# Kernel optimization log

Measured on AMD Instinct MI355X. Metric: run time of the kernel, lower is better.

## Reference

```python
import jax, jax.numpy as jnp
import numpy as np

N, D_IN, D_H, D_ATT, N_CLUSTERS, N_CLASSES = 20000, 1024, 512, 256, 10, 4


def setup_inputs() -> dict:
    key = jax.random.key(0)
    ks = jax.random.split(key, 20)
    s = 0.02
    inp = {
        "x_path": jax.random.normal(ks[0], (N, D_IN), dtype=jnp.float32),
        "cluster_id": jax.random.randint(ks[1], (N,), 0, N_CLUSTERS, dtype=jnp.int64 if jax.config.jax_enable_x64 else jnp.int32),
        # per-cluster expert MLPs (phi_i): 1024->512->512
        "W1": jax.random.normal(ks[2], (N_CLUSTERS, D_IN, D_H), dtype=jnp.float32) * s,
        "b1": jnp.zeros((N_CLUSTERS, D_H), dtype=jnp.float32),
        "W2": jax.random.normal(ks[3], (N_CLUSTERS, D_H, D_H), dtype=jnp.float32) * s,
        "b2": jnp.zeros((N_CLUSTERS, D_H), dtype=jnp.float32),
        # attention_net: fc (512->512) then gated attention (L=512, D=256, 1)
        "Wfc": jax.random.normal(ks[4], (D_H, D_H), dtype=jnp.float32) * s,
        "bfc": jnp.zeros((D_H,), dtype=jnp.float32),
        "Wa": jax.random.normal(ks[5], (D_H, D_ATT), dtype=jnp.float32) * s,
        "ba": jnp.zeros((D_ATT,), dtype=jnp.float32),
        "Wb": jax.random.normal(ks[6], (D_H, D_ATT), dtype=jnp.float32) * s,
        "bb": jnp.zeros((D_ATT,), dtype=jnp.float32),
        "Wc": jax.random.normal(ks[7], (D_ATT, 1), dtype=jnp.float32) * s,
        "bc": jnp.zeros((1,), dtype=jnp.float32),
        # rho: 512->256
        "Wrho": jax.random.normal(ks[8], (D_H, D_ATT), dtype=jnp.float32) * s,
        "brho": jnp.zeros((D_ATT,), dtype=jnp.float32),
        # classifier: 256->4
        "Wcls": jax.random.normal(ks[9], (D_ATT, N_CLASSES), dtype=jnp.float32) * s,
        "bcls": jnp.zeros((N_CLASSES,), dtype=jnp.float32),
    }
    return inp


def reference(x_path, cluster_id, W1, b1, W2, b2, Wfc, bfc, Wa, ba, Wb, bb, Wc, bc, Wrho, brho, Wcls, bcls):
    C = W1.shape[0]
    # dispatch mask [N, C]; per-cluster counts
    onehot = jax.nn.one_hot(cluster_id, C, dtype=x_path.dtype)
    counts = jnp.maximum(onehot.sum(axis=0), 1.0)  # [C]
    # per-cluster expert MLP + masked mean-pool (AdaptiveAvgPool1d(1) over instances)
    pooled = []
    for i in range(C):  # small static loop over experts
        h = jax.nn.relu(x_path @ W1[i] + b1[i])      # [N, 512]
        h = jax.nn.relu(h @ W2[i] + b2[i])           # [N, 512]
        pooled.append((onehot[:, i] @ h) / counts[i])  # masked mean -> [512]
    h_cluster = jnp.stack(pooled, axis=0)            # [C, 512]
    # attention_net: fc then gated attention
    h = jax.nn.relu(h_cluster @ Wfc + bfc)           # [C, 512]
    a = jnp.tanh(h @ Wa + ba)                        # [C, 256]
    b = jax.nn.sigmoid(h @ Wb + bb)                  # [C, 256]
    A = ((a * b) @ Wc + bc).T                        # [1, C]
    A = jax.nn.softmax(A, axis=1)
    h_path = A @ h                                   # [1, 512]
    h_path = jax.nn.relu(h_path @ Wrho + brho).squeeze()  # [256]
    logits = (h_path @ Wcls + bcls)[None, :]         # [1, 4]
    Y_hat = jnp.argmax(logits, axis=1, keepdims=True)
    hazards = jax.nn.sigmoid(logits)
    S = jnp.cumprod(1.0 - hazards, axis=1)
    return hazards, S, Y_hat
```

## Files before the change

kernel.cpp:

```cpp
#include <hip/hip_runtime.h>
#include <hip/hip_bf16.h>
#include <math.h>


#define C_NUM 10
#define D_IN 1024
#define D_H 512
#define D_ATT 256
#define N_CLS 4
#define BM 128
#define BMG 64
#define BN 128
#define BKS 64
#define NT1 (D_IN / BKS)
#define NT2 (D_H / BKS)

typedef __attribute__((ext_vector_type(8))) short short8v;
typedef __attribute__((ext_vector_type(4))) short short4v;
typedef __attribute__((ext_vector_type(4))) float f32x4;

__device__ __forceinline__ short f2bf(float f) {
    __hip_bfloat16 h = __float2bfloat16(f);
    return *reinterpret_cast<short*>(&h);
}

__device__ __forceinline__ void gload_lds16(const void* g, void* l) {
    __builtin_amdgcn_global_load_lds((const __attribute__((address_space(1))) unsigned int*)g,
                                     (__attribute__((address_space(3))) unsigned int*)l,
                                     16, 0, 0);
}

__device__ __forceinline__ int xcd_swizzle(int orig, int nwg) {
    int q = nwg >> 3, r = nwg & 7;
    int xcd = orig & 7, base = orig >> 3;
    return (xcd < r ? xcd * (q + 1) : r * (q + 1) + (xcd - r) * q) + base;
}

__global__ __launch_bounds__(256) void k_hist(const int* __restrict__ cid, int* counts, int n) {
    __shared__ int lc[C_NUM];
    int tid = threadIdx.x;
    if (tid < C_NUM) lc[tid] = 0;
    __syncthreads();
    int i = blockIdx.x * 256 + tid;
    if (i < n) atomicAdd(&lc[cid[i]], 1);
    __syncthreads();
    if (tid < C_NUM && lc[tid] > 0) atomicAdd(&counts[tid], lc[tid]);
}

__global__ __launch_bounds__(256) void k_scatter(const int* __restrict__ cid, int* cursor,
                                                 const int* __restrict__ counts,
                                                 int* bucket, int n) {
    __shared__ int lc[C_NUM];
    __shared__ int basev[C_NUM];
    __shared__ int loff[C_NUM + 1];
    int tid = threadIdx.x;
    if (tid < C_NUM) lc[tid] = 0;
    if (tid == 0) {
        int off = 0;
        for (int c2 = 0; c2 < C_NUM; ++c2) {
            loff[c2] = off;
            off += ((counts[c2] + BM - 1) / BM) * BM;
        }
        loff[C_NUM] = off;
    }
    __syncthreads();
    int i = blockIdx.x * 256 + tid;
    int c = 0, lpos = 0;
    bool valid = (i < n);
    if (valid) { c = cid[i]; lpos = atomicAdd(&lc[c], 1); }
    __syncthreads();
    if (tid < C_NUM) basev[tid] = (lc[tid] > 0) ? atomicAdd(&cursor[tid], lc[tid]) : 0;
    __syncthreads();
    if (valid) bucket[loff[c] + basev[c] + lpos] = i;
    if (blockIdx.x == 0) {
        for (int c2 = 0; c2 < C_NUM; ++c2)
            for (int p = loff[c2] + counts[c2] + tid; p < loff[c2 + 1]; p += 256)
                bucket[p] = -1;
    }
}

__global__ __launch_bounds__(256) void k_transpose2(
    const float* __restrict__ W1, short* __restrict__ Wt1,
    const float* __restrict__ W2, short* __restrict__ Wt2)
{
    __shared__ float t[64][65];
    int bid = blockIdx.x;
    const float* src; short* dst; int K, N, k0, n0;
    if (bid < C_NUM * 128) {
        int cc = bid >> 7, r = bid & 127;
        k0 = (r & 15) * 64; n0 = (r >> 4) * 64;
        src = W1 + (size_t)cc * D_IN * D_H; dst = Wt1 + (size_t)cc * D_H * D_IN;
        K = D_IN; N = D_H;
    } else {
        int idx = bid - C_NUM * 128;
        int cc = idx >> 6, r = idx & 63;
        k0 = (r & 7) * 64; n0 = (r >> 3) * 64;
        src = W2 + (size_t)cc * D_H * D_H; dst = Wt2 + (size_t)cc * D_H * D_H;
        K = D_H; N = D_H;
    }
    int tid = threadIdx.x;
    int tk = tid >> 4, tn4 = (tid & 15) * 4;
#pragma unroll
    for (int it = 0; it < 4; ++it) {
        int k = tk + it * 16;
        f32x4 v = *(const f32x4*)&src[(size_t)(k0 + k) * N + n0 + tn4];
        t[k][tn4 + 0] = v[0]; t[k][tn4 + 1] = v[1];
        t[k][tn4 + 2] = v[2]; t[k][tn4 + 3] = v[3];
    }
    __syncthreads();
    int wn = tid >> 2, kq = (tid & 3) * 16;
#pragma unroll
    for (int q = 0; q < 4; ++q) {
        int k = kq + q * 4;
        short4v o;
#pragma unroll
        for (int e = 0; e < 4; ++e) o[e] = f2bf(t[k + e][wn]);
        *(short4v*)&dst[(size_t)(n0 + wn) * K + k0 + k] = o;
    }
}

__global__ __launch_bounds__(512) void k_gemm1w(
    const float* __restrict__ x, const short* __restrict__ Wt, const float* __restrict__ b1,
    const int* __restrict__ bucket, const int* __restrict__ counts, short* __restrict__ h1)
{
    __shared__ float Asf[BMG * BKS];
    __shared__ short Bs[BN * BKS];
    __shared__ int ridx[BMG];
    __shared__ int saoff[C_NUM + 1];

    int tid = threadIdx.x;
    int wg = xcd_swizzle(blockIdx.x, gridDim.x);
    int rowStart = (wg >> 2) * BMG;
    int colStart = (wg & 3) * BN;

    if (tid == 0) {
        int off = 0;
        for (int c2 = 0; c2 < C_NUM; ++c2) {
            saoff[c2] = off;
            off += ((counts[c2] + BM - 1) / BM) * BM;
        }
        saoff[C_NUM] = off;
    }
    if (tid < BMG) ridx[tid] = bucket[rowStart + tid];
    __syncthreads();
    if (rowStart >= saoff[C_NUM]) return;
    int c = 0;
    while (c < C_NUM - 1 && rowStart >= saoff[c + 1]) ++c;

    int lane = tid & 63;
    int wid = tid >> 6;
    int wm = wid >> 2;
    int wn = wid & 3;

    const float* aq[2];
#pragma unroll
    for (int q = 0; q < 2; ++q) {
        int row = q * 32 + wid * 4 + (lane >> 4);
        int rr = ridx[row];
        int srcslot = (lane & 15) ^ (row & 15);
        aq[q] = x + (size_t)(rr < 0 ? 0 : rr) * D_IN + srcslot * 4;
    }
    int l8 = lane >> 3;
    int sslot = (lane & 7) ^ l8;
    const short* bq[2];
#pragma unroll
    for (int q = 0; q < 2; ++q) {
        int rowb = q * 64 + wid * 8 + l8;
        bq[q] = Wt + ((size_t)c * D_H + colStart + rowb) * D_IN + sslot * 8;
    }

    f32x4 acc[2][2];
#pragma unroll
    for (int i = 0; i < 2; ++i)
#pragma unroll
        for (int j = 0; j < 2; ++j)
            acc[i][j] = f32x4{0.f, 0.f, 0.f, 0.f};

    for (int k0 = 0; k0 < D_IN; k0 += BKS) {
        gload_lds16(bq[0] + k0, &Bs[(wid * 8) * BKS]);
        gload_lds16(bq[1] + k0, &Bs[(64 + wid * 8) * BKS]);
        gload_lds16(aq[0] + k0, &Asf[(wid * 4) * BKS]);
        gload_lds16(aq[1] + k0, &Asf[(32 + wid * 4) * BKS]);
        __syncthreads();
#pragma unroll
        for (int kk = 0; kk < 2; ++kk) {
            short8v af[2], bfr[2];
#pragma unroll
            for (int i = 0; i < 2; ++i) {
                int row = wm * 32 + i * 16 + (lane & 15);
                int s8 = kk * 4 + (lane >> 4);
                int p0 = (2 * s8) ^ (row & 15);
                int p1 = (2 * s8 + 1) ^ (row & 15);
                f32x4 lo = *(const f32x4*)&Asf[row * BKS + p0 * 4];
                f32x4 hi = *(const f32x4*)&Asf[row * BKS + p1 * 4];
                short8v v;
#pragma unroll
                for (int e = 0; e < 4; ++e) { v[e] = f2bf(lo[e]); v[4 + e] = f2bf(hi[e]); }
                af[i] = v;
            }
#pragma unroll
            for (int j = 0; j < 2; ++j) {
                int nn = wn * 32 + j * 16 + (lane & 15);
                int slot = (kk * 4 + (lane >> 4)) ^ (nn & 7);
                bfr[j] = *(const short8v*)&Bs[nn * BKS + slot * 8];
            }
#pragma unroll
            for (int i = 0; i < 2; ++i)
#pragma unroll
                for (int j = 0; j < 2; ++j)
                    acc[i][j] = __builtin_amdgcn_mfma_f32_16x16x32_bf16(af[i], bfr[j], acc[i][j], 0, 0, 0);
        }
        __syncthreads();
    }

    const float* bias = b1 + c * D_H;
    float bj[2];
#pragma unroll
    for (int j = 0; j < 2; ++j) bj[j] = bias[colStart + wn * 32 + j * 16 + (lane & 15)];
#pragma unroll
    for (int i = 0; i < 2; ++i) {
#pragma unroll
        for (int r = 0; r < 4; ++r) {
            int rowl = wm * 32 + i * 16 + (lane >> 4) * 4 + r;
            bool valid = (ridx[rowl] >= 0);
            size_t gro = (size_t)(rowStart + rowl) * D_H + colStart + wn * 32 + (lane & 15);
#pragma unroll
            for (int j = 0; j < 2; ++j) {
                float v = valid ? fmaxf(acc[i][j][r] + bj[j], 0.f) : 0.f;
                h1[gro + j * 16] = f2bf(v);
            }
        }
    }
}

__global__ __launch_bounds__(512) void k_gemm2w(
    const short* __restrict__ h1, const short* __restrict__ Wt, const float* __restrict__ b2,
    const int* __restrict__ bucket, const int* __restrict__ counts, float* __restrict__ pooled)
{
    __shared__ short As[BMG * BKS];
    __shared__ short Bs[BN * BKS];
    __shared__ int ridx[BMG];
    __shared__ int saoff[C_NUM + 1];

    int tid = threadIdx.x;
    int wg = xcd_swizzle(blockIdx.x, gridDim.x);
    int rowStart = (wg >> 2) * BMG;
    int colStart = (wg & 3) * BN;

    if (tid == 0) {
        int off = 0;
        for (int c2 = 0; c2 < C_NUM; ++c2) {
            saoff[c2] = off;
            off += ((counts[c2] + BM - 1) / BM) * BM;
        }
        saoff[C_NUM] = off;
    }
    if (tid < BMG) ridx[tid] = bucket[rowStart + tid];
    __syncthreads();
    if (rowStart >= saoff[C_NUM]) return;
    int c = 0;
    while (c < C_NUM - 1 && rowStart >= saoff[c + 1]) ++c;

    int lane = tid & 63;
    int wid = tid >> 6;
    int wm = wid >> 2, wn = wid & 3;

    int l8 = lane >> 3;
    int sslot = (lane & 7) ^ l8;
    const short* abase = h1 + (size_t)(rowStart + wid * 8 + l8) * D_H + sslot * 8;
    const short* bq[2];
#pragma unroll
    for (int q = 0; q < 2; ++q) {
        int rowb = q * 64 + wid * 8 + l8;
        bq[q] = Wt + ((size_t)c * D_H + colStart + rowb) * D_H + sslot * 8;
    }

    f32x4 acc[2][2];
#pragma unroll
    for (int i = 0; i < 2; ++i)
#pragma unroll
        for (int j = 0; j < 2; ++j)
            acc[i][j] = f32x4{0.f, 0.f, 0.f, 0.f};

    for (int k0 = 0; k0 < D_H; k0 += BKS) {
        gload_lds16(abase + k0, &As[(wid * 8) * BKS]);
        gload_lds16(bq[0] + k0, &Bs[(wid * 8) * BKS]);
        gload_lds16(bq[1] + k0, &Bs[(64 + wid * 8) * BKS]);
        __syncthreads();
#pragma unroll
        for (int kk = 0; kk < 2; ++kk) {
            short8v af[2], bfr[2];
#pragma unroll
            for (int i = 0; i < 2; ++i) {
                int row = wm * 32 + i * 16 + (lane & 15);
                int slot = (kk * 4 + (lane >> 4)) ^ (row & 7);
                af[i] = *(const short8v*)&As[row * BKS + slot * 8];
            }
#pragma unroll
            for (int j = 0; j < 2; ++j) {
                int nn = wn * 32 + j * 16 + (lane & 15);
                int slot = (kk * 4 + (lane >> 4)) ^ (nn & 7);
                bfr[j] = *(const short8v*)&Bs[nn * BKS + slot * 8];
            }
#pragma unroll
            for (int i = 0; i < 2; ++i)
#pragma unroll
                for (int j = 0; j < 2; ++j)
                    acc[i][j] = __builtin_amdgcn_mfma_f32_16x16x32_bf16(af[i], bfr[j], acc[i][j], 0, 0, 0);
        }
        __syncthreads();
    }

    const float* bias = b2 + c * D_H;
    float bj[2];
#pragma unroll
    for (int j = 0; j < 2; ++j) bj[j] = bias[colStart + wn * 32 + j * 16 + (lane & 15)];
    float csum[2] = {0.f, 0.f};
#pragma unroll
    for (int i = 0; i < 2; ++i) {
#pragma unroll
        for (int r = 0; r < 4; ++r) {
            int rowl = wm * 32 + i * 16 + (lane >> 4) * 4 + r;
            float m = (ridx[rowl] >= 0) ? 1.f : 0.f;
#pragma unroll
            for (int j = 0; j < 2; ++j)
                csum[j] += m * fmaxf(acc[i][j][r] + bj[j], 0.f);
        }
    }
#pragma unroll
    for (int j = 0; j < 2; ++j) {
        float s = csum[j];
        s += __shfl_xor(s, 16, 64);
        s += __shfl_xor(s, 32, 64);
        if ((lane >> 4) == 0)
            atomicAdd(&pooled[c * D_H + colStart + wn * 32 + j * 16 + lane], s);
    }
}

__global__ __launch_bounds__(256) void k_tA(
    const float* __restrict__ pooled, const int* __restrict__ counts,
    const float* __restrict__ Wfc, const float* __restrict__ bfc,
    float* __restrict__ hfc)
{
    __shared__ float hcs[C_NUM][D_H];
    __shared__ float red[4][64][C_NUM];
    int tid = threadIdx.x;
    for (int idx = tid; idx < C_NUM * D_H; idx += 256) {
        int cc = idx >> 9;
        hcs[cc][idx & (D_H - 1)] = pooled[idx] / fmaxf((float)counts[cc], 1.f);
    }
    __syncthreads();
    int col = blockIdx.x * 64 + (tid & 63);
    int kq = tid >> 6, k0 = kq * 128;
    float acc[C_NUM] = {};
    for (int k = 0; k < 128; ++k) {
        float wv = Wfc[(size_t)(k0 + k) * D_H + col];
#pragma unroll
        for (int cc = 0; cc < C_NUM; ++cc) acc[cc] += hcs[cc][k0 + k] * wv;
    }
#pragma unroll
    for (int cc = 0; cc < C_NUM; ++cc) red[kq][tid & 63][cc] = acc[cc];
    __syncthreads();
    if (kq == 0) {
        float bv = bfc[col];
#pragma unroll
        for (int cc = 0; cc < C_NUM; ++cc) {
            float s = red[0][tid][cc] + red[1][tid][cc] + red[2][tid][cc] + red[3][tid][cc];
            hfc[cc * D_H + col] = fmaxf(s + bv, 0.f);
        }
    }
}

__global__ __launch_bounds__(256) void k_tB(
    const float* __restrict__ hfc,
    const float* __restrict__ Wa, const float* __restrict__ ba,
    const float* __restrict__ Wb, const float* __restrict__ bb,
    const float* __restrict__ Wc,
    float* __restrict__ scores)
{
    __shared__ float hfs[C_NUM][D_H];
    __shared__ float red[4][64][C_NUM][2];
    int tid = threadIdx.x;
    for (int idx = tid; idx < C_NUM * D_H; idx += 256) {
        hfs[idx >> 9][idx & (D_H - 1)] = hfc[idx];
    }
    __syncthreads();
    int ad = blockIdx.x * 64 + (tid & 63);
    int kq = tid >> 6, k0 = kq * 128;
    float sa[C_NUM] = {}, sb[C_NUM] = {};
    for (int k = 0; k < 128; ++k) {
        float wav = Wa[(size_t)(k0 + k) * D_ATT + ad];
        float wbv = Wb[(size_t)(k0 + k) * D_ATT + ad];
#pragma unroll
        for (int cc = 0; cc < C_NUM; ++cc) {
            float h = hfs[cc][k0 + k];
            sa[cc] += h * wav;
            sb[cc] += h * wbv;
        }
    }
#pragma unroll
    for (int cc = 0; cc < C_NUM; ++cc) {
        red[kq][tid & 63][cc][0] = sa[cc];
        red[kq][tid & 63][cc][1] = sb[cc];
    }
    __syncthreads();
    if (kq == 0) {
        float bav = ba[ad], bbv = bb[ad], wcv = Wc[ad];
#pragma unroll
        for (int cc = 0; cc < C_NUM; ++cc) {
            float sat = red[0][tid][cc][0] + red[1][tid][cc][0] + red[2][tid][cc][0] + red[3][tid][cc][0];
            float sbt = red[0][tid][cc][1] + red[1][tid][cc][1] + red[2][tid][cc][1] + red[3][tid][cc][1];
            float v = tanhf(sat + bav) * (1.f / (1.f + expf(-(sbt + bbv)))) * wcv;
            v += __shfl_xor(v, 1, 64); v += __shfl_xor(v, 2, 64); v += __shfl_xor(v, 4, 64);
            v += __shfl_xor(v, 8, 64); v += __shfl_xor(v, 16, 64); v += __shfl_xor(v, 32, 64);
            if (tid == 0) atomicAdd(&scores[cc], v);
        }
    }
}

__global__ __launch_bounds__(256) void k_tCDE(
    const float* __restrict__ scores, const float* __restrict__ bc,
    const float* __restrict__ hfc, const float* __restrict__ Wrho,
    float* __restrict__ hr_raw, int* __restrict__ done,
    const float* __restrict__ brho,
    const float* __restrict__ Wcls, const float* __restrict__ bcls,
    float* __restrict__ out)
{
    __shared__ float hps[32];
    __shared__ int amLast;
    int tid = threadIdx.x;
    int k0 = blockIdx.x * 32;
    if (tid < 32) {
        float sc2[C_NUM];
        float mx = -1e30f;
#pragma unroll
        for (int cc = 0; cc < C_NUM; ++cc) { sc2[cc] = scores[cc] + bc[0]; mx = fmaxf(mx, sc2[cc]); }
        float sum = 0.f;
#pragma unroll
        for (int cc = 0; cc < C_NUM; ++cc) { sc2[cc] = expf(sc2[cc] - mx); sum += sc2[cc]; }
        float s = 0.f;
#pragma unroll
        for (int cc = 0; cc < C_NUM; ++cc) s += (sc2[cc] / sum) * hfc[cc * D_H + k0 + tid];
        hps[tid] = s;
    }
    __syncthreads();
    float acc = 0.f;
#pragma unroll 8
    for (int k = 0; k < 32; ++k)
        acc += hps[k] * Wrho[(size_t)(k0 + k) * D_ATT + tid];
    atomicAdd(&hr_raw[tid], acc);

    __threadfence();
    if (tid == 0) amLast = (atomicAdd(done, 1) == (int)gridDim.x - 1);
    __syncthreads();
    if (!amLast) return;

    __shared__ float cpart[4][N_CLS];
    int lane = tid & 63, w = tid >> 6;
    float hraw = atomicAdd(&hr_raw[tid], 0.f);
    float h = fmaxf(hraw + brho[tid], 0.f);
    f32x4 wv = *(const f32x4*)&Wcls[tid * N_CLS];
    float v[N_CLS];
#pragma unroll
    for (int l = 0; l < N_CLS; ++l) {
        v[l] = h * wv[l];
        v[l] += __shfl_xor(v[l], 1, 64); v[l] += __shfl_xor(v[l], 2, 64);
        v[l] += __shfl_xor(v[l], 4, 64); v[l] += __shfl_xor(v[l], 8, 64);
        v[l] += __shfl_xor(v[l], 16, 64); v[l] += __shfl_xor(v[l], 32, 64);
    }
    if (lane == 0) {
#pragma unroll
        for (int l = 0; l < N_CLS; ++l) cpart[w][l] = v[l];
    }
    __syncthreads();
    if (tid == 0) {
        float lg[N_CLS];
#pragma unroll
        for (int l = 0; l < N_CLS; ++l)
            lg[l] = cpart[0][l] + cpart[1][l] + cpart[2][l] + cpart[3][l] + bcls[l];
        int best = 0;
#pragma unroll
        for (int l = 1; l < N_CLS; ++l) if (lg[l] > lg[best]) best = l;
        float Sv = 1.f;
#pragma unroll
        for (int l = 0; l < N_CLS; ++l) {
            float hz = 1.f / (1.f + expf(-lg[l]));
            out[l] = hz;
            Sv *= (1.f - hz);
            out[4 + l] = Sv;
        }
        out[8] = (float)best;
    }
}

extern "C" void kernel_launch(void* const* d_in, const int* in_sizes, int n_in,
                              void* d_out, int out_size, void* d_ws, size_t ws_size,
                              hipStream_t stream)
{
    const float* x    = (const float*)d_in[0];
    const int*   cid  = (const int*)d_in[1];
    const float* W1   = (const float*)d_in[2];
    const float* b1   = (const float*)d_in[3];
    const float* W2   = (const float*)d_in[4];
    const float* b2   = (const float*)d_in[5];
    const float* Wfc  = (const float*)d_in[6];
    const float* bfc  = (const float*)d_in[7];
    const float* Wa   = (const float*)d_in[8];
    const float* ba   = (const float*)d_in[9];
    const float* Wb   = (const float*)d_in[10];
    const float* bb   = (const float*)d_in[11];
    const float* Wc   = (const float*)d_in[12];
    const float* bc   = (const float*)d_in[13];
    const float* Wrho = (const float*)d_in[14];
    const float* brho = (const float*)d_in[15];
    const float* Wcls = (const float*)d_in[16];
    const float* bcls = (const float*)d_in[17];
    float* out = (float*)d_out;

    int n = in_sizes[0] / D_IN;
    int rowTiles = (n + BM - 1) / BM + C_NUM;
    int npadMax = rowTiles * BM;
    int rowTiles64 = rowTiles * 2;

    char* w = (char*)d_ws;
    int* counts   = (int*)w;
    int* cursor   = counts + 16;
    float* scores = (float*)(counts + 32);
    int* done     = (int*)(scores + 16);
    float* hr_raw = (float*)(done + 16);
    float* pooled = hr_raw + 256;
    size_t zero_bytes = (size_t)(16 + 16 + 16 + 16 + 256 + 5120) * 4;
    float* hfc  = pooled + 5120;
    int* bucket = (int*)(hfc + 5120);
    short* Wt1 = (short*)(bucket + npadMax);
    short* Wt2 = Wt1 + (size_t)C_NUM * D_H * D_IN;
    short* h1  = Wt2 + (size_t)C_NUM * D_H * D_H;

    hipMemsetAsync(w, 0, zero_bytes, stream);

    int nb = (n + 255) / 256;
    k_hist<<<nb, 256, 0, stream>>>(cid, counts, n);
    k_scatter<<<nb, 256, 0, stream>>>(cid, cursor, counts, bucket, n);

    k_transpose2<<<C_NUM * 128 + C_NUM * 64, 256, 0, stream>>>(W1, Wt1, W2, Wt2);

    k_gemm1w<<<rowTiles64 * 4, 512, 0, stream>>>(x, Wt1, b1, bucket, counts, h1);
    k_gemm2w<<<rowTiles64 * 4, 512, 0, stream>>>(h1, Wt2, b2, bucket, counts, pooled);

    k_tA<<<8, 256, 0, stream>>>(pooled, counts, Wfc, bfc, hfc);
    k_tB<<<4, 256, 0, stream>>>(hfc, Wa, ba, Wb, bb, Wc, scores);
    k_tCDE<<<16, 256, 0, stream>>>(scores, bc, hfc, Wrho, hr_raw, done,
                                   brho, Wcls, bcls, out);
}
```

Measured before the change: 126.3 us.

## Pre-convert x to bf16 and use bf16 LDS-direct A loads in GEMM1

Adds a pass that converts x from fp32 to bf16 in a workspace buffer, plus a new GEMM1 kernel that streams bf16 A tiles straight into LDS with global_load_lds instead of staging fp32 and converting. This halves the A-tile bytes per GEMM tile, and each x row is read four times (once per column block). The cost is an extra full pass over x (read 80MB, write 40MB) and more workspace. The old path is kept as a fallback when the workspace is too small.

```diff
diff --git a/kernel.cpp b/kernel.cpp
--- a/kernel.cpp
+++ b/kernel.cpp
@@ -12,8 +12,6 @@
 #define BMG 64
 #define BN 128
 #define BKS 64
-#define NT1 (D_IN / BKS)
-#define NT2 (D_H / BKS)
 
 typedef __attribute__((ext_vector_type(8))) short short8v;
 typedef __attribute__((ext_vector_type(4))) short short4v;
@@ -77,6 +75,17 @@
             for (int p = loff[c2] + counts[c2] + tid; p < loff[c2 + 1]; p += 256)
                 bucket[p] = -1;
     }
+}
+
+__global__ __launch_bounds__(256) void k_convertlin(const float* __restrict__ x,
+                                                    short* __restrict__ xbl) {
+    size_t i = (size_t)blockIdx.x * 256 + threadIdx.x;
+    const f32x4* p = (const f32x4*)(x + i * 8);
+    f32x4 f0 = p[0], f1 = p[1];
+    short8v v;
+#pragma unroll
+    for (int e = 0; e < 4; ++e) { v[e] = f2bf(f0[e]); v[4 + e] = f2bf(f1[e]); }
+    *(short8v*)&xbl[i * 8] = v;
 }
 
 __global__ __launch_bounds__(256) void k_transpose2(
@@ -119,11 +128,11 @@
     }
 }
 
-__global__ __launch_bounds__(512) void k_gemm1w(
-    const float* __restrict__ x, const short* __restrict__ Wt, const float* __restrict__ b1,
+__global__ __launch_bounds__(512) void k_gemm1b5(
+    const short* __restrict__ xbl, const short* __restrict__ Wt, const float* __restrict__ b1,
     const int* __restrict__ bucket, const int* __restrict__ counts, short* __restrict__ h1)
 {
-    __shared__ float Asf[BMG * BKS];
+    __shared__ short As[BMG * BKS];
     __shared__ short Bs[BN * BKS];
     __shared__ int ridx[BMG];
     __shared__ int saoff[C_NUM + 1];
@@ -151,6 +160,106 @@
     int wid = tid >> 6;
     int wm = wid >> 2;
     int wn = wid & 3;
+
+    int l8 = lane >> 3;
+    int sslot = (lane & 7) ^ l8;
+    int arow = wid * 8 + l8;
+    int rr = ridx[arow];
+    const short* abase = xbl + (size_t)(rr < 0 ? 0 : rr) * D_IN + sslot * 8;
+    const short* bq[2];
+#pragma unroll
+    for (int q = 0; q < 2; ++q) {
+        int rowb = q * 64 + wid * 8 + l8;
+        bq[q] = Wt + ((size_t)c * D_H + colStart + rowb) * D_IN + sslot * 8;
+    }
+
+    f32x4 acc[2][2];
+#pragma unroll
+    for (int i = 0; i < 2; ++i)
+#pragma unroll
+        for (int j = 0; j < 2; ++j)
+            acc[i][j] = f32x4{0.f, 0.f, 0.f, 0.f};
+
+    for (int k0 = 0; k0 < D_IN; k0 += BKS) {
+        gload_lds16(abase + k0, &As[(wid * 8) * BKS]);
+        gload_lds16(bq[0] + k0, &Bs[(wid * 8) * BKS]);
+        gload_lds16(bq[1] + k0, &Bs[(64 + wid * 8) * BKS]);
+        __syncthreads();
+#pragma unroll
+        for (int kk = 0; kk < 2; ++kk) {
+            short8v af[2], bfr[2];
+#pragma unroll
+            for (int i = 0; i < 2; ++i) {
+                int row = wm * 32 + i * 16 + (lane & 15);
+                int slot = (kk * 4 + (lane >> 4)) ^ (row & 7);
+                af[i] = *(const short8v*)&As[row * BKS + slot * 8];
+            }
+#pragma unroll
+            for (int j = 0; j < 2; ++j) {
+                int nn = wn * 32 + j * 16 + (lane & 15);
+                int slot = (kk * 4 + (lane >> 4)) ^ (nn & 7);
+                bfr[j] = *(const short8v*)&Bs[nn * BKS + slot * 8];
+            }
+#pragma unroll
+            for (int i = 0; i < 2; ++i)
+#pragma unroll
+                for (int j = 0; j < 2; ++j)
+                    acc[i][j] = __builtin_amdgcn_mfma_f32_16x16x32_bf16(af[i], bfr[j], acc[i][j], 0, 0, 0);
+        }
+        __syncthreads();
+    }
+
+    const float* bias = b1 + c * D_H;
+    float bj[2];
+#pragma unroll
+    for (int j = 0; j < 2; ++j) bj[j] = bias[colStart + wn * 32 + j * 16 + (lane & 15)];
+#pragma unroll
+    for (int i = 0; i < 2; ++i) {
+#pragma unroll
+        for (int r = 0; r < 4; ++r) {
+            int rowl = wm * 32 + i * 16 + (lane >> 4) * 4 + r;
+            bool valid = (ridx[rowl] >= 0);
+            size_t gro = (size_t)(rowStart + rowl) * D_H + colStart + wn * 32 + (lane & 15);
+#pragma unroll
+            for (int j = 0; j < 2; ++j) {
+                float v = valid ? fmaxf(acc[i][j][r] + bj[j], 0.f) : 0.f;
+                h1[gro + j * 16] = f2bf(v);
+            }
+        }
+    }
+}
+
+__global__ __launch_bounds__(512) void k_gemm1w(
+    const float* __restrict__ x, const short* __restrict__ Wt, const float* __restrict__ b1,
+    const int* __restrict__ bucket, const int* __restrict__ counts, short* __restrict__ h1)
+{
+    __shared__ float Asf[BMG * BKS];
+    __shared__ short Bs[BN * BKS];
+    __shared__ int ridx[BMG];
+    __shared__ int saoff[C_NUM + 1];
+
+    int tid = threadIdx.x;
+    int wg = xcd_swizzle(blockIdx.x, gridDim.x);
+    int rowStart = (wg >> 2) * BMG;
+    int colStart = (wg & 3) * BN;
+
+    if (tid == 0) {
+        int off = 0;
+        for (int c2 = 0; c2 < C_NUM; ++c2) {
+            saoff[c2] = off;
+            off += ((counts[c2] + BM - 1) / BM) * BM;
+        }
+        saoff[C_NUM] = off;
+    }
+    if (tid < BMG) ridx[tid] = bucket[rowStart + tid];
+    __syncthreads();
+    if (rowStart >= saoff[C_NUM]) return;
+    int c = 0;
+    while (c < C_NUM - 1 && rowStart >= saoff[c + 1]) ++c;
+
+    int lane = tid & 63;
+    int wid = tid >> 6;
+    int wm = wid >> 2, wn = wid & 3;
 
     const float* aq[2];
 #pragma unroll
@@ -535,6 +644,9 @@
     short* Wt1 = (short*)(bucket + npadMax);
     short* Wt2 = Wt1 + (size_t)C_NUM * D_H * D_IN;
     short* h1  = Wt2 + (size_t)C_NUM * D_H * D_H;
+    short* xbl = h1 + (size_t)npadMax * D_H;
+    size_t need_big = (size_t)((char*)(xbl + (size_t)n * D_IN) - w);
+    bool big = ws_size >= need_big;
 
     hipMemsetAsync(w, 0, zero_bytes, stream);
 
@@ -544,7 +656,12 @@
 
     k_transpose2<<<C_NUM * 128 + C_NUM * 64, 256, 0, stream>>>(W1, Wt1, W2, Wt2);
 
-    k_gemm1w<<<rowTiles64 * 4, 512, 0, stream>>>(x, Wt1, b1, bucket, counts, h1);
+    if (big) {
+        k_convertlin<<<(n * D_IN / 8 + 255) / 256, 256, 0, stream>>>(x, xbl);
+        k_gemm1b5<<<rowTiles64 * 4, 512, 0, stream>>>(xbl, Wt1, b1, bucket, counts, h1);
+    } else {
+        k_gemm1w<<<rowTiles64 * 4, 512, 0, stream>>>(x, Wt1, b1, bucket, counts, h1);
+    }
     k_gemm2w<<<rowTiles64 * 4, 512, 0, stream>>>(h1, Wt2, b2, bucket, counts, pooled);
 
     k_tA<<<8, 256, 0, stream>>>(pooled, counts, Wfc, bfc, hfc);
```

After: 135.1 us. +6.9%, slower.
